# Optimization experiments

Measured on AMD Instinct MI355X. Metric: run time of the kernel, lower is better.

## Reference

```python
import jax, jax.numpy as jnp
import numpy as np
import math

DIM, DIM_QK, DIM_V = 1024, 128, 1024
NUM_BUCKETS, MAX_DISTANCE = 32, 128


def silu(x):
    return x * jax.nn.sigmoid(x)


def laplacian_attn_fn(x):
    mu = math.sqrt(0.5)
    std = math.sqrt(0.25 * math.pi)
    return (1.0 + jax.lax.erf((x - mu) / (std * math.sqrt(2.0)))) * 0.5


def rel_pos_bias(seq_len, table, scale):
    # causal T5 bucketing: n = q_pos - k_pos, clamped at 0
    q_pos = jnp.arange(seq_len)
    k_pos = jnp.arange(seq_len)
    rel_pos = k_pos[None, :] - q_pos[:, None]  # [i, j]
    n = jnp.maximum(-rel_pos, 0)
    max_exact = NUM_BUCKETS // 2
    is_small = n < max_exact
    n_safe = jnp.maximum(n, 1).astype(jnp.float32)
    val_if_large = max_exact + (
        jnp.log(n_safe / max_exact) / math.log(MAX_DISTANCE / max_exact)
        * (NUM_BUCKETS - max_exact)
    ).astype(jnp.int32)
    val_if_large = jnp.minimum(val_if_large, NUM_BUCKETS - 1)
    bucket = jnp.where(is_small, n, val_if_large)
    return table[bucket] * scale  # [i, j]


def setup_inputs() -> dict:
    key = jax.random.key(0)
    ks = jax.random.split(key, 8)
    B, S = 4, 2048
    lin_std_qk = 1.0 / math.sqrt(DIM)
    return {
        "x": jax.random.normal(ks[0], (B, S, DIM), dtype=jnp.float32),
        "wqk": jax.random.uniform(ks[1], (DIM, DIM_QK), minval=-lin_std_qk, maxval=lin_std_qk, dtype=jnp.float32),
        "bqk": jnp.zeros((DIM_QK,), dtype=jnp.float32),
        "gamma": 1.0 + 0.02 * jax.random.normal(ks[2], (2, DIM_QK), dtype=jnp.float32),
        "beta": jnp.zeros((2, DIM_QK), dtype=jnp.float32),
        "wv": jax.random.uniform(ks[3], (DIM, DIM_V), minval=-lin_std_qk, maxval=lin_std_qk, dtype=jnp.float32),
        "bv": jnp.zeros((DIM_V,), dtype=jnp.float32),
        "rel_bias": jax.random.normal(ks[4], (NUM_BUCKETS,), dtype=jnp.float32),
    }


def reference(x, wqk, bqk, gamma, beta, wv, bv, rel_bias):
    B, S, _ = x.shape
    qk = silu(x @ wqk + bqk)                       # [B, S, dqk]
    q = qk * gamma[0] + beta[0]
    k = qk * gamma[1] + beta[1]
    v = silu(x @ wv + bv)                          # [B, S, dv]
    scale = 1.0 / S                                # laplacian_attn_fn scaling
    sim = jnp.einsum('bid,bjd->bij', q, k) * scale
    sim = sim + rel_pos_bias(S, rel_bias, DIM_QK ** 0.5)[None, :, :]
    attn = laplacian_attn_fn(sim)
    causal_mask = jnp.triu(jnp.ones((S, S), dtype=bool), k=1)
    attn = jnp.where(causal_mask[None, :, :], 0.0, attn)
    return jnp.einsum('bij,bjd->bid', attn, v)
```

## Files before the change

kernel.cpp:

```cpp
#include <hip/hip_runtime.h>
#include <stdint.h>


#define B_   4
#define S_   2048
#define DIM_ 1024
#define DQK  128
#define DV   1024
#define NQV  1152

typedef __attribute__((ext_vector_type(8))) short short8;
typedef __attribute__((ext_vector_type(4))) float f32x4;

__device__ __forceinline__ uint16_t f32_to_bf16(float f) {
  uint32_t u = __float_as_uint(f);
  u += 0x7FFFu + ((u >> 16) & 1u);
  return (uint16_t)(u >> 16);
}

__device__ __forceinline__ uint32_t pack_bf16(float a, float b) {
  return (uint32_t)f32_to_bf16(a) | ((uint32_t)f32_to_bf16(b) << 16);
}

__device__ __forceinline__ float silu_f(float x) {
  return x * __builtin_amdgcn_rcpf(1.0f + __expf(-x));
}

__device__ __forceinline__ float laplacian_attn(float x) {
  float z  = (x - 0.70710678118654752f) * 0.79788456080286536f;
  float az = fabsf(z);
  float t  = __builtin_amdgcn_rcpf(fmaf(0.3275911f, az, 1.0f));
  float w  = fmaf(1.061405429f, t, -1.453152027f);
  w = fmaf(w, t, 1.421413741f);
  w = fmaf(w, t, -0.284496736f);
  w = fmaf(w, t, 0.254829592f);
  float P  = w * t;
  float E  = __expf(-z * z);
  float ea = fmaf(-P, E, 1.0f);
  float er = copysignf(ea, z);
  return fmaf(0.5f, er, 0.5f);
}

template <int MT, int NT, int DEPTH>
__device__ __forceinline__ void wave_gemm_t(
    const uint16_t* __restrict__ A, int KBa, int rbA,
    const uint16_t* __restrict__ Bt, int KBb, int rbB,
    int nkb, f32x4 acc[MT][NT])
{
  const int lane = threadIdx.x & 63;

  const uint16_t* pa[MT];
  const uint16_t* pb[NT];
  #pragma unroll
  for (int mt = 0; mt < MT; mt++)
    pa[mt] = A + (size_t)(rbA + mt) * KBa * 512 + lane * 8;
  #pragma unroll
  for (int nt = 0; nt < NT; nt++)
    pb[nt] = Bt + (size_t)(rbB + nt) * KBb * 512 + lane * 8;

  #pragma unroll
  for (int mt = 0; mt < MT; mt++)
    #pragma unroll
    for (int nt = 0; nt < NT; nt++) {
      f32x4 z = {0.0f, 0.0f, 0.0f, 0.0f};
      acc[mt][nt] = z;
    }

  short8 fa0[MT], fb0[NT], fa1[MT], fb1[NT];

  auto loads = [&](short8 fa[MT], short8 fb[NT], int kb) {
    #pragma unroll
    for (int mt = 0; mt < MT; mt++)
      fa[mt] = *(const short8*)(pa[mt] + (size_t)kb * 512);
    #pragma unroll
    for (int nt = 0; nt < NT; nt++)
      fb[nt] = *(const short8*)(pb[nt] + (size_t)kb * 512);
  };
  auto mfmas = [&](short8 fa[MT], short8 fb[NT]) {
    #pragma unroll
    for (int mt = 0; mt < MT; mt++)
      #pragma unroll
      for (int nt = 0; nt < NT; nt++)
        acc[mt][nt] = __builtin_amdgcn_mfma_f32_16x16x32_bf16(
            fa[mt], fb[nt], acc[mt][nt], 0, 0, 0);
  };

  if constexpr (DEPTH == 2) {
    loads(fa0, fb0, 0);
    loads(fa1, fb1, 1);
    for (int kb = 2; kb < nkb; kb += 2) {
      mfmas(fa0, fb0);
      loads(fa0, fb0, kb);
      mfmas(fa1, fb1);
      loads(fa1, fb1, kb + 1);
    }
    mfmas(fa0, fb0);
    mfmas(fa1, fb1);
  } else {
    short8 fa2[MT], fb2[NT], fa3[MT], fb3[NT];
    loads(fa0, fb0, 0);
    loads(fa1, fb1, 1);
    loads(fa2, fb2, 2);
    loads(fa3, fb3, 3);
    for (int kb = 4; kb < nkb; kb += 4) {
      mfmas(fa0, fb0);
      loads(fa0, fb0, kb);
      mfmas(fa1, fb1);
      loads(fa1, fb1, kb + 1);
      mfmas(fa2, fb2);
      loads(fa2, fb2, kb + 2);
      mfmas(fa3, fb3);
      loads(fa3, fb3, kb + 3);
    }
    mfmas(fa0, fb0);
    mfmas(fa1, fb1);
    mfmas(fa2, fb2);
    mfmas(fa3, fb3);
  }
}

#define WAVE_PREAMBLE                                  \
  int lane = threadIdx.x & 63;                         \
  int wave = threadIdx.x >> 6;                         \
  int lane16 = lane & 15;                              \
  int quad = lane >> 4;                                \
  int wrow = (wave >> 1) * 64;                         \
  int wcol = (wave & 1) * 64;

__global__ __launch_bounds__(256) void k_prep(
    const float* __restrict__ x, const float* __restrict__ wqk,
    const float* __restrict__ wv, const float* __restrict__ rel,
    uint16_t* __restrict__ xb, uint16_t* __restrict__ wT,
    float* __restrict__ bias_n)
{
  int blk = blockIdx.x;
  if (blk < 4096) {
    int t = blk * 256 + threadIdx.x;
    int i16 = t & 15, oct = (t >> 4) & 3, kb = (t >> 6) & 31, ib = t >> 11;
    const float* src = x + (size_t)(ib * 16 + i16) * DIM_ + kb * 32 + oct * 8;
    float4 a = *(const float4*)src;
    float4 b = *(const float4*)(src + 4);
    short8 o;
    o[0] = f32_to_bf16(a.x); o[1] = f32_to_bf16(a.y);
    o[2] = f32_to_bf16(a.z); o[3] = f32_to_bf16(a.w);
    o[4] = f32_to_bf16(b.x); o[5] = f32_to_bf16(b.y);
    o[6] = f32_to_bf16(b.z); o[7] = f32_to_bf16(b.w);
    *(short8*)(xb + (size_t)t * 8) = o;
  } else if (blk < 4672) {
    int t = (blk - 4096) * 256 + threadIdx.x;
    int n16 = t & 15, oct = (t >> 4) & 3, kb = (t >> 6) & 31, nb = t >> 11;
    int n = nb * 16 + n16;
    int k0 = kb * 32 + oct * 8;
    short8 o;
    if (n < DQK) {
      #pragma unroll
      for (int j = 0; j < 8; j++)
        o[j] = f32_to_bf16(wqk[(size_t)(k0 + j) * DQK + n]);
    } else {
      int nn = n - DQK;
      #pragma unroll
      for (int j = 0; j < 8; j++)
        o[j] = f32_to_bf16(wv[(size_t)(k0 + j) * DV + nn]);
    }
    *(short8*)(wT + (size_t)t * 8) = o;
  } else {
    for (int n = threadIdx.x; n < S_; n += 256) {
      int bucket;
      if (n < 16) {
        bucket = n;
      } else {
        float tt = logf((float)n * 0.0625f) / 2.0794415416798357f * 16.0f;
        int vl = 16 + (int)tt;
        bucket = vl < 31 ? vl : 31;
      }
      bias_n[n] = rel[bucket] * 11.313708498984761f;
    }
  }
}


__global__ __launch_bounds__(256, 3) void k_gemm_qkv(
    const uint16_t* __restrict__ xb, const uint16_t* __restrict__ wT,
    const float* __restrict__ bqk, const float* __restrict__ gamma,
    const float* __restrict__ beta, const float* __restrict__ bv,
    uint16_t* __restrict__ qb, uint16_t* __restrict__ kb,
    uint16_t* __restrict__ vT)
{
  int L = blockIdx.x;
  int c = L & 7;
  int idx = L >> 3;
  int by = c + 8 * (idx / 9);
  int bx = idx % 9;
  WAVE_PREAMBLE
  f32x4 acc[4][4];

  if (bx == 0) {
    wave_gemm_t<4,4,2>(wT, DIM_ >> 5, (wave >> 1) * 4,
                       xb, DIM_ >> 5, by * 8 + (wave & 1) * 4,
                       DIM_ >> 5, acc);
    int ibase = by * 128 + (wave & 1) * 64;
    int cbase = (wave >> 1) * 64;
    #pragma unroll
    for (int mt = 0; mt < 4; mt++) {
      int c0 = cbase + mt * 16 + quad * 4;
      float4 bb = *(const float4*)(bqk + c0);
      float4 g0 = *(const float4*)(gamma + c0);
      float4 g1 = *(const float4*)(gamma + DQK + c0);
      float4 e0 = *(const float4*)(beta + c0);
      float4 e1 = *(const float4*)(beta + DQK + c0);
      size_t coff = (size_t)(c0 >> 5) * 512 + ((c0 >> 3) & 3) * 128 + (c0 & 7);
      #pragma unroll
      for (int nt = 0; nt < 4; nt++) {
        int i = ibase + nt * 16 + lane16;
        float s0 = silu_f(acc[mt][nt][0] + bb.x);
        float s1 = silu_f(acc[mt][nt][1] + bb.y);
        float s2 = silu_f(acc[mt][nt][2] + bb.z);
        float s3 = silu_f(acc[mt][nt][3] + bb.w);
        uint2 pq, pk;
        pq.x = pack_bf16(fmaf(s0, g0.x, e0.x), fmaf(s1, g0.y, e0.y));
        pq.y = pack_bf16(fmaf(s2, g0.z, e0.z), fmaf(s3, g0.w, e0.w));
        pk.x = pack_bf16(fmaf(s0, g1.x, e1.x), fmaf(s1, g1.y, e1.y));
        pk.y = pack_bf16(fmaf(s2, g1.z, e1.z), fmaf(s3, g1.w, e1.w));
        size_t off = (size_t)(i >> 4) * 4 * 512 + (size_t)(i & 15) * 8 + coff;
        *(uint2*)(qb + off) = pq;
        *(uint2*)(kb + off) = pk;
      }
    }
  } else {
    wave_gemm_t<4,4,2>(xb, DIM_ >> 5, by * 8 + (wave >> 1) * 4,
                       wT, DIM_ >> 5, bx * 8 + (wave & 1) * 4,
                       DIM_ >> 5, acc);
    int b = by >> 4;
    uint16_t* vt = vT + (size_t)b * DV * S_;
    #pragma unroll
    for (int nt = 0; nt < 4; nt++) {
      int n = (bx - 1) * 128 + wcol + nt * 16 + lane16;
      float bb = bv[n];
      #pragma unroll
      for (int mt = 0; mt < 4; mt++) {
        int j0l = (by & 15) * 128 + wrow + mt * 16 + quad * 4;
        uint16_t v0 = f32_to_bf16(silu_f(acc[mt][nt][0] + bb));
        uint16_t v1 = f32_to_bf16(silu_f(acc[mt][nt][1] + bb));
        uint16_t v2 = f32_to_bf16(silu_f(acc[mt][nt][2] + bb));
        uint16_t v3 = f32_to_bf16(silu_f(acc[mt][nt][3] + bb));
        size_t off = (size_t)((n >> 4) * 64 + (j0l >> 5)) * 512 +
                     ((j0l >> 3) & 3) * 128 + (n & 15) * 8 + (j0l & 7);
        uint2 pk;
        pk.x = (uint32_t)v0 | ((uint32_t)v1 << 16);
        pk.y = (uint32_t)v2 | ((uint32_t)v3 << 16);
        *(uint2*)(vt + off) = pk;
      }
    }
  }
}

__global__ __launch_bounds__(128, 4) void k_gemm_sim(
    const uint16_t* __restrict__ qb, const uint16_t* __restrict__ kb,
    const float* __restrict__ bias_n, uint16_t* __restrict__ attn)
{
  int b = blockIdx.x;
  int bt = blockIdx.y;
  int it = (int)((sqrtf(8.0f * (float)b + 1.0f) - 1.0f) * 0.5f);
  while ((it + 1) * (it + 2) / 2 <= b) ++it;
  while (it * (it + 1) / 2 > b) --it;
  int jt = b - it * (it + 1) / 2;

  int lane = threadIdx.x & 63;
  int wave = threadIdx.x >> 6;
  int lane16 = lane & 15;
  int quad = lane >> 4;

  f32x4 acc[4][2];
  wave_gemm_t<4,2,2>(kb, 4, bt * 128 + jt * 4,
                     qb, 4, bt * 128 + it * 4 + wave * 2,
                     4, acc);

  uint16_t* ab = attn + (size_t)bt * S_ * S_;
  int ibase = it * 64 + wave * 32;
  int jbase = jt * 64;
  #pragma unroll
  for (int nt = 0; nt < 2; nt++) {
    int i = ibase + nt * 16 + lane16;
    size_t irow = (size_t)(i >> 4) * 64 * 512 + (size_t)(i & 15) * 8;
    #pragma unroll
    for (int mt = 0; mt < 4; mt++) {
      int j0 = jbase + mt * 16 + quad * 4;
      float v[4];
      #pragma unroll
      for (int r = 0; r < 4; r++) {
        int j = j0 + r;
        float aval = 0.0f;
        if (j <= i) {
          float sim = acc[mt][nt][r] * (1.0f / 2048.0f) + bias_n[i - j];
          aval = laplacian_attn(sim);
        }
        v[r] = aval;
      }
      uint2 pk;
      pk.x = pack_bf16(v[0], v[1]);
      pk.y = pack_bf16(v[2], v[3]);
      size_t off = irow + (size_t)(j0 >> 5) * 512 + ((j0 >> 3) & 3) * 128 +
                   (j0 & 7);
      *(uint2*)(ab + off) = pk;
    }
  }
}

__global__ __launch_bounds__(256, 2) void k_gemm_out(
    const uint16_t* __restrict__ attn, const uint16_t* __restrict__ vT,
    float* __restrict__ out)
{
  int L = blockIdx.x;
  int c = L & 7, m = L >> 3;
  int bt = c >> 1;
  int nx = (c & 1) * 4 + (m & 3);
  int it = 15 - (m >> 2);
  int nkb = 4 * it + 4;
  WAVE_PREAMBLE
  f32x4 acc[4][4];
  wave_gemm_t<4,4,4>(vT + (size_t)bt * DV * S_, 64, nx * 8 + (wave & 1) * 4,
                     attn + (size_t)bt * S_ * S_, 64, it * 8 + (wave >> 1) * 4,
                     nkb, acc);
  float* ob = out + ((size_t)bt * S_ + it * 128 + wrow) * DV + nx * 128 + wcol;
  #pragma unroll
  for (int nt = 0; nt < 4; nt++) {
    int i = nt * 16 + lane16;
    #pragma unroll
    for (int mt = 0; mt < 4; mt++) {
      int n = mt * 16 + quad * 4;
      *(float4*)(ob + (size_t)i * DV + n) = *(float4*)&acc[mt][nt];
    }
  }
}


extern "C" void kernel_launch(void* const* d_in, const int* in_sizes, int n_in,
                              void* d_out, int out_size, void* d_ws, size_t ws_size,
                              hipStream_t stream)
{
  const float* x     = (const float*)d_in[0];
  const float* wqk   = (const float*)d_in[1];
  const float* bqk   = (const float*)d_in[2];
  const float* gamma = (const float*)d_in[3];
  const float* beta  = (const float*)d_in[4];
  const float* wv    = (const float*)d_in[5];
  const float* bv    = (const float*)d_in[6];
  const float* rel   = (const float*)d_in[7];
  float* out = (float*)d_out;

  char* ws = (char*)d_ws;
  size_t off = 0;
  uint16_t* xb     = (uint16_t*)(ws + off); off += (size_t)B_ * S_ * DIM_ * 2;
  uint16_t* wT     = (uint16_t*)(ws + off); off += (size_t)NQV * DIM_ * 2;
  uint16_t* qb     = (uint16_t*)(ws + off); off += (size_t)B_ * S_ * DQK * 2;
  uint16_t* kb     = (uint16_t*)(ws + off); off += (size_t)B_ * S_ * DQK * 2;
  uint16_t* vT     = (uint16_t*)(ws + off); off += (size_t)B_ * DV * S_ * 2;
  uint16_t* attn   = (uint16_t*)(ws + off); off += (size_t)B_ * S_ * S_ * 2;
  float*    bias_n = (float*)(ws + off);    off += (size_t)S_ * 4;

  k_prep<<<dim3(4673), dim3(256), 0, stream>>>(x, wqk, wv, rel, xb, wT, bias_n);

  k_gemm_qkv<<<dim3(576), dim3(256), 0, stream>>>(
      xb, wT, bqk, gamma, beta, bv, qb, kb, vT);
  k_gemm_sim<<<dim3(528, B_), dim3(128), 0, stream>>>(
      qb, kb, bias_n, attn);
  k_gemm_out<<<dim3(512), dim3(256), 0, stream>>>(
      attn, vT, out);
}
```

Measured before the change: 172.9 us.

## Stage GEMM operand tiles through LDS with direct global-to-LDS loads

The QKV projection and output GEMMs now use global_load_lds to copy each block's A and B fragment tiles into shared memory once, and waves read their fragments from LDS. Before, each wave loaded its fragments straight from global memory with no sharing across waves. This cuts redundant global and L2 traffic, but the schedule is single-buffered with two barriers per k-step, so loads no longer overlap the MFMAs. The output GEMM's occupancy hint is also raised from 2 to 3 blocks per CU, and the depth-4 path of the register-prefetch helper is dropped.

Measured after the change: 171.0 us. No clear change (-1.1%).

```diff
diff --git a/kernel.cpp b/kernel.cpp
--- a/kernel.cpp
+++ b/kernel.cpp
@@ -41,6 +41,12 @@
   return fmaf(0.5f, er, 0.5f);
 }
 
+__device__ __forceinline__ void gload16(const uint16_t* g, uint16_t* l) {
+  __builtin_amdgcn_global_load_lds(
+      (const __attribute__((address_space(1))) void*)g,
+      (__attribute__((address_space(3))) void*)l, 16, 0, 0);
+}
+
 template <int MT, int NT, int DEPTH>
 __device__ __forceinline__ void wave_gemm_t(
     const uint16_t* __restrict__ A, int KBa, int rbA,
@@ -85,38 +91,16 @@
             fa[mt], fb[nt], acc[mt][nt], 0, 0, 0);
   };
 
-  if constexpr (DEPTH == 2) {
-    loads(fa0, fb0, 0);
-    loads(fa1, fb1, 1);
-    for (int kb = 2; kb < nkb; kb += 2) {
-      mfmas(fa0, fb0);
-      loads(fa0, fb0, kb);
-      mfmas(fa1, fb1);
-      loads(fa1, fb1, kb + 1);
-    }
+  loads(fa0, fb0, 0);
+  loads(fa1, fb1, 1);
+  for (int kb = 2; kb < nkb; kb += 2) {
     mfmas(fa0, fb0);
+    loads(fa0, fb0, kb);
     mfmas(fa1, fb1);
-  } else {
-    short8 fa2[MT], fb2[NT], fa3[MT], fb3[NT];
-    loads(fa0, fb0, 0);
-    loads(fa1, fb1, 1);
-    loads(fa2, fb2, 2);
-    loads(fa3, fb3, 3);
-    for (int kb = 4; kb < nkb; kb += 4) {
-      mfmas(fa0, fb0);
-      loads(fa0, fb0, kb);
-      mfmas(fa1, fb1);
-      loads(fa1, fb1, kb + 1);
-      mfmas(fa2, fb2);
-      loads(fa2, fb2, kb + 2);
-      mfmas(fa3, fb3);
-      loads(fa3, fb3, kb + 3);
-    }
-    mfmas(fa0, fb0);
-    mfmas(fa1, fb1);
-    mfmas(fa2, fb2);
-    mfmas(fa3, fb3);
-  }
+    loads(fa1, fb1, kb + 1);
+  }
+  mfmas(fa0, fb0);
+  mfmas(fa1, fb1);
 }
 
 #define WAVE_PREAMBLE                                  \
@@ -192,12 +176,55 @@
   int by = c + 8 * (idx / 9);
   int bx = idx % 9;
   WAVE_PREAMBLE
+
+  __shared__ uint16_t sA[8 * 2 * 512];
+  __shared__ uint16_t sB[8 * 2 * 512];
+
+  const uint16_t *Ab, *Bb;
+  if (bx == 0) { Ab = wT;                              Bb = xb + (size_t)by * 8 * 32 * 512; }
+  else         { Ab = xb + (size_t)by * 8 * 32 * 512;  Bb = wT + (size_t)bx * 8 * 32 * 512; }
+
+  const uint16_t* gp = (wave >> 1) ? Bb : Ab;
+  uint16_t*       sp = (wave >> 1) ? sB : sA;
+  int rb0 = (wave & 1) * 4;
+
   f32x4 acc[4][4];
+  #pragma unroll
+  for (int mt = 0; mt < 4; mt++)
+    #pragma unroll
+    for (int nt = 0; nt < 4; nt++) {
+      f32x4 z = {0.0f, 0.0f, 0.0f, 0.0f};
+      acc[mt][nt] = z;
+    }
+
+  for (int kbi = 0; kbi < 32; kbi += 2) {
+    #pragma unroll
+    for (int uu = 0; uu < 8; uu++) {
+      int rbu = rb0 + (uu >> 1), kk = uu & 1;
+      gload16(gp + ((size_t)rbu * 32 + kbi + kk) * 512 + lane * 8,
+              sp + (rbu * 2 + kk) * 512);
+    }
+    __syncthreads();
+    #pragma unroll
+    for (int kk = 0; kk < 2; kk++) {
+      short8 fa[4], fb[4];
+      #pragma unroll
+      for (int mt = 0; mt < 4; mt++)
+        fa[mt] = *(const short8*)(sA + (((wave >> 1) * 4 + mt) * 2 + kk) * 512 + lane * 8);
+      #pragma unroll
+      for (int nt = 0; nt < 4; nt++)
+        fb[nt] = *(const short8*)(sB + (((wave & 1) * 4 + nt) * 2 + kk) * 512 + lane * 8);
+      #pragma unroll
+      for (int mt = 0; mt < 4; mt++)
+        #pragma unroll
+        for (int nt = 0; nt < 4; nt++)
+          acc[mt][nt] = __builtin_amdgcn_mfma_f32_16x16x32_bf16(
+              fa[mt], fb[nt], acc[mt][nt], 0, 0, 0);
+    }
+    __syncthreads();
+  }
 
   if (bx == 0) {
-    wave_gemm_t<4,4,2>(wT, DIM_ >> 5, (wave >> 1) * 4,
-                       xb, DIM_ >> 5, by * 8 + (wave & 1) * 4,
-                       DIM_ >> 5, acc);
     int ibase = by * 128 + (wave & 1) * 64;
     int cbase = (wave >> 1) * 64;
     #pragma unroll
@@ -227,9 +254,6 @@
       }
     }
   } else {
-    wave_gemm_t<4,4,2>(xb, DIM_ >> 5, by * 8 + (wave >> 1) * 4,
-                       wT, DIM_ >> 5, bx * 8 + (wave & 1) * 4,
-                       DIM_ >> 5, acc);
     int b = by >> 4;
     uint16_t* vt = vT + (size_t)b * DV * S_;
     #pragma unroll
@@ -306,7 +330,7 @@
   }
 }
 
-__global__ __launch_bounds__(256, 2) void k_gemm_out(
+__global__ __launch_bounds__(256, 3) void k_gemm_out(
     const uint16_t* __restrict__ attn, const uint16_t* __restrict__ vT,
     float* __restrict__ out)
 {
@@ -317,10 +341,53 @@
   int it = 15 - (m >> 2);
   int nkb = 4 * it + 4;
   WAVE_PREAMBLE
+
+  __shared__ uint16_t sA[8 * 2 * 512];
+  __shared__ uint16_t sB[8 * 2 * 512];
+
+  const uint16_t* Ab = vT + (size_t)bt * DV * S_ + (size_t)nx * 8 * 64 * 512;
+  const uint16_t* Bb = attn + (size_t)bt * S_ * S_ + (size_t)it * 8 * 64 * 512;
+
+  const uint16_t* gp = (wave >> 1) ? Bb : Ab;
+  uint16_t*       sp = (wave >> 1) ? sB : sA;
+  int rb0 = (wave & 1) * 4;
+
   f32x4 acc[4][4];
-  wave_gemm_t<4,4,4>(vT + (size_t)bt * DV * S_, 64, nx * 8 + (wave & 1) * 4,
-                     attn + (size_t)bt * S_ * S_, 64, it * 8 + (wave >> 1) * 4,
-                     nkb, acc);
+  #pragma unroll
+  for (int mt = 0; mt < 4; mt++)
+    #pragma unroll
+    for (int nt = 0; nt < 4; nt++) {
+      f32x4 z = {0.0f, 0.0f, 0.0f, 0.0f};
+      acc[mt][nt] = z;
+    }
+
+  for (int kbi = 0; kbi < nkb; kbi += 2) {
+    #pragma unroll
+    for (int uu = 0; uu < 8; uu++) {
+      int rbu = rb0 + (uu >> 1), kk = uu & 1;
+      gload16(gp + ((size_t)rbu * 64 + kbi + kk) * 512 + lane * 8,
+              sp + (rbu * 2 + kk) * 512);
+    }
+    __syncthreads();
+    #pragma unroll
+    for (int kk = 0; kk < 2; kk++) {
+      short8 fa[4], fb[4];
+      #pragma unroll
+      for (int mt = 0; mt < 4; mt++)
+        fa[mt] = *(const short8*)(sA + (((wave & 1) * 4 + mt) * 2 + kk) * 512 + lane * 8);
+      #pragma unroll
+      for (int nt = 0; nt < 4; nt++)
+        fb[nt] = *(const short8*)(sB + (((wave >> 1) * 4 + nt) * 2 + kk) * 512 + lane * 8);
+      #pragma unroll
+      for (int mt = 0; mt < 4; mt++)
+        #pragma unroll
+        for (int nt = 0; nt < 4; nt++)
+          acc[mt][nt] = __builtin_amdgcn_mfma_f32_16x16x32_bf16(
+              fa[mt], fb[nt], acc[mt][nt], 0, 0, 0);
+    }
+    __syncthreads();
+  }
+
   float* ob = out + ((size_t)bt * S_ + it * 128 + wrow) * DV + nx * 128 + wcol;
   #pragma unroll
   for (int nt = 0; nt < 4; nt++) {
```
